# Kernel optimization log

Measured on AMD Instinct MI355X. Metric: run time of the kernel, lower is better.

Reference implementation:

```python
import jax, jax.numpy as jnp
import numpy as np

HEAD_NUM = 16
EMBED = 1024
B, T = 2, 2048


def setup_inputs() -> dict:
    key = jax.random.key(0)
    k1, k2, k3 = jax.random.split(key, 3)
    x = jax.random.normal(k1, (B, T, EMBED), dtype=jnp.float32)
    # torch Linear weights: [out_features, in_features]; scaled like default init
    w_qkv = jax.random.normal(k2, (3 * EMBED, EMBED), dtype=jnp.float32) / np.sqrt(EMBED)
    w_out = jax.random.normal(k3, (EMBED, EMBED), dtype=jnp.float32) / np.sqrt(EMBED)
    return {"x": x, "w_qkv": w_qkv, "w_out": w_out}


def reference(x, w_qkv, w_out):
    b, t, e = x.shape
    h = HEAD_NUM
    d = e // h
    dk = d ** 0.5  # NOTE: original MULTIPLIES scores by sqrt(head_dim)
    qkv = x @ w_qkv.T  # [b, t, 3e]
    # einops 'b t (d k h) -> k b h t d' with k=3: split order is (d, 3, h)
    qkv = qkv.reshape(b, t, d, 3, h)
    qkv = jnp.transpose(qkv, (3, 0, 4, 1, 2))  # [3, b, h, t, d]
    q, k, v = qkv[0], qkv[1], qkv[2]
    energy = jnp.einsum('bhid,bhjd->bhij', q, k) * dk  # [b, h, t, t]
    attn = jax.nn.softmax(energy, axis=-1)
    out = jnp.einsum('bhij,bhjd->bhid', attn, v)  # [b, h, t, d]
    out = jnp.transpose(out, (0, 2, 1, 3)).reshape(b, t, e)  # b t (h d)
    return out @ w_out.T
```

## Files before the change

kernel.cpp:

```cpp
#include <hip/hip_runtime.h>
#include <hip/hip_bf16.h>

typedef _Float16 f16x8 __attribute__((ext_vector_type(8)));
typedef unsigned short u16x8 __attribute__((ext_vector_type(8)));
typedef unsigned short u16x4 __attribute__((ext_vector_type(4)));
typedef float f32x4 __attribute__((ext_vector_type(4)));

static constexpr int Bn = 2;
static constexpr int Tn = 2048;
static constexpr int En = 1024;
static constexpr int Hn = 16;
static constexpr int Dn = 64;
#define LOG2E 1.44269504088896340736f

static constexpr int TS = 136;
static constexpr int PS = 40;

__device__ __forceinline__ unsigned short f2h(float x) {
  _Float16 h = (_Float16)x;
  return __builtin_bit_cast(unsigned short, h);
}
__device__ __forceinline__ float h2f(unsigned short u) {
  return (float)__builtin_bit_cast(_Float16, u);
}
__device__ __forceinline__ f16x8 ldh8(const unsigned short* p) {
  return __builtin_bit_cast(f16x8, *reinterpret_cast<const u16x8*>(p));
}
__device__ __forceinline__ unsigned int pk2(float a, float b) {
  return __builtin_bit_cast(unsigned int, __builtin_amdgcn_cvt_pkrtz(a, b));
}
__device__ __forceinline__ float fexp2(float x) {
  return __builtin_amdgcn_exp2f(x);
}
__device__ __forceinline__ void gld16(const void* g, void* l) {
  __builtin_amdgcn_global_load_lds(
      (__attribute__((address_space(1))) void*)(const_cast<void*>(g)),
      (__attribute__((address_space(3))) void*)(l), 16, 0, 0);
}

__global__ __launch_bounds__(256) void split_f32_f16(
    const float* __restrict__ src, unsigned short* __restrict__ hi,
    unsigned short* __restrict__ lo)
{
  const int i = (blockIdx.x * 256 + threadIdx.x) * 4;
  const float4 v = *reinterpret_cast<const float4*>(src + i);
  ushort4 h, l;
  h.x = f2h(v.x); l.x = f2h(v.x - h2f(h.x));
  h.y = f2h(v.y); l.y = f2h(v.y - h2f(h.y));
  h.z = f2h(v.z); l.z = f2h(v.z - h2f(h.z));
  h.w = f2h(v.w); l.w = f2h(v.w - h2f(h.w));
  *reinterpret_cast<ushort4*>(hi + i) = h;
  *reinterpret_cast<ushort4*>(lo + i) = l;
}

__global__ __launch_bounds__(256) void cvt_f32_f16(
    const float* __restrict__ src, unsigned short* __restrict__ dst)
{
  const int i = (blockIdx.x * 256 + threadIdx.x) * 4;
  const float4 v = *reinterpret_cast<const float4*>(src + i);
  ushort4 u;
  u.x = f2h(v.x); u.y = f2h(v.y); u.z = f2h(v.z); u.w = f2h(v.w);
  *reinterpret_cast<ushort4*>(dst + i) = u;
}

__global__ __launch_bounds__(256) void gemm_qkv(
    const unsigned short* __restrict__ xh, const unsigned short* __restrict__ xl,
    const unsigned short* __restrict__ wf,
    unsigned short* __restrict__ Qf, unsigned short* __restrict__ Kf,
    unsigned short* __restrict__ Vf, int M, int K)
{
  __shared__ unsigned short smem[2 * 12288];

  const int tid = threadIdx.x;
  const int w = tid >> 6, L = tid & 63, qd = L >> 4, lr = L & 15;
  const int m0 = blockIdx.y * 128;
  const int kk = blockIdx.x >> 3;
  const int hh0 = (blockIdx.x & 7) * 2;
  const int wm = (w >> 1) * 64, wn = (w & 1) * 64;

  size_t aoffs[2], boffs[2];
  int lbase[2];
#pragma unroll
  for (int p = 0; p < 2; ++p) {
    const int c = p * 256 + tid;
    const int row = c >> 2, slot = c & 3;
    const int dd = row & 63, hl = row >> 6;
    const int sg = slot ^ ((row >> 1) & 3);
    aoffs[p] = (size_t)(m0 + row) * K + sg * 8;
    boffs[p] = (size_t)(dd * 48 + kk * 16 + hh0 + hl) * K + sg * 8;
    lbase[p] = (p * 4 + w) * 512;
  }

  f32x4 acc[4][4] = {};

#pragma unroll
  for (int p = 0; p < 2; ++p) {
    gld16(xh + aoffs[p], &smem[lbase[p]]);
    gld16(wf + boffs[p], &smem[8192 + lbase[p]]);
    if (kk < 2) gld16(xl + aoffs[p], &smem[4096 + lbase[p]]);
  }
  __syncthreads();

  const int sw = (qd ^ ((lr >> 1) & 3)) * 8;

  int buf = 0;
  for (int k0 = 0; k0 < K; k0 += 32) {
    if (k0 + 32 < K) {
      const int nb = (buf ^ 1) * 12288;
#pragma unroll
      for (int p = 0; p < 2; ++p) {
        gld16(xh + aoffs[p] + k0 + 32, &smem[nb + lbase[p]]);
        gld16(wf + boffs[p] + k0 + 32, &smem[nb + 8192 + lbase[p]]);
        if (kk < 2) gld16(xl + aoffs[p] + k0 + 32, &smem[nb + 4096 + lbase[p]]);
      }
    }

    const int cb = buf * 12288;
    f16x8 afh[4], bf[4];
#pragma unroll
    for (int mt = 0; mt < 4; ++mt)
      afh[mt] = ldh8(&smem[cb + (wm + mt * 16 + lr) * 32 + sw]);
#pragma unroll
    for (int nt = 0; nt < 4; ++nt)
      bf[nt] = ldh8(&smem[cb + 8192 + (wn + nt * 16 + lr) * 32 + sw]);
    if (kk < 2) {
      f16x8 afl[4];
#pragma unroll
      for (int mt = 0; mt < 4; ++mt)
        afl[mt] = ldh8(&smem[cb + 4096 + (wm + mt * 16 + lr) * 32 + sw]);
#pragma unroll
      for (int mt = 0; mt < 4; ++mt)
#pragma unroll
        for (int nt = 0; nt < 4; ++nt) {
          acc[mt][nt] = __builtin_amdgcn_mfma_f32_16x16x32_f16(afh[mt], bf[nt], acc[mt][nt], 0, 0, 0);
          acc[mt][nt] = __builtin_amdgcn_mfma_f32_16x16x32_f16(afl[mt], bf[nt], acc[mt][nt], 0, 0, 0);
        }
    } else {
#pragma unroll
      for (int mt = 0; mt < 4; ++mt)
#pragma unroll
        for (int nt = 0; nt < 4; ++nt)
          acc[mt][nt] = __builtin_amdgcn_mfma_f32_16x16x32_f16(afh[mt], bf[nt], acc[mt][nt], 0, 0, 0);
    }
    __syncthreads();
    buf ^= 1;
  }

  const int b = m0 >> 11;
  const int t0 = m0 & (Tn - 1);
  const float qscale = (kk == 0) ? 8.0f * LOG2E : 1.0f;
#pragma unroll
  for (int mt = 0; mt < 4; ++mt)
#pragma unroll
    for (int nt = 0; nt < 4; ++nt)
#pragma unroll
      for (int r = 0; r < 4; ++r) {
        const int ml = wm + mt * 16 + qd * 4 + r;
        const int cl = wn + nt * 16 + lr;
        smem[ml * TS + cl] = f2h(acc[mt][nt][r] * qscale);
      }
  __syncthreads();

  unsigned short* dst = (kk == 0) ? Qf : (kk == 1) ? Kf : Vf;
  if (kk < 2) {
#pragma unroll
    for (int p = 0; p < 8; ++p) {
      const int s = p * 256 + tid;
      const int tl = s >> 4, sub = s & 15;
      const int hl = sub >> 3, oct = sub & 7;
      const u16x8 v = *reinterpret_cast<const u16x8*>(&smem[tl * TS + hl * 64 + oct * 8]);
      *reinterpret_cast<u16x8*>(
          dst + ((size_t)(b * Hn + hh0 + hl) * Tn + t0 + tl) * Dn + oct * 8) = v;
    }
  } else {
#pragma unroll
    for (int p = 0; p < 8; ++p) {
      const int s = p * 256 + tid;
      const int cl = s >> 4, oct = s & 15;
      const int hl = cl >> 6, dd = cl & 63;
      u16x8 v;
#pragma unroll
      for (int j = 0; j < 8; ++j) v[j] = smem[(oct * 8 + j) * TS + cl];
      *reinterpret_cast<u16x8*>(
          dst + ((size_t)((b * Hn + hh0 + hl) * Dn + dd)) * Tn + t0 + oct * 8) = v;
    }
  }
}

__global__ __launch_bounds__(256, 2) void attn_kernel(
    const unsigned short* __restrict__ Qf, const unsigned short* __restrict__ Kf,
    const unsigned short* __restrict__ Vf, unsigned short* __restrict__ AOf)
{
  __shared__ unsigned short shK[2 * 128 * 32];
  __shared__ unsigned short shV[4 * 64 * 32];
  __shared__ unsigned short shP[4 * 16 * PS];
  const int tid = threadIdx.x;
  const int w = tid >> 6, L = tid & 63, qd = L >> 4, lr = L & 15;
  const int q0 = blockIdx.x * 64;
  const int bh = blockIdx.y;
  unsigned short* myP = &shP[w * 16 * PS];

  f16x8 aq[2];
  {
    const size_t qoff = ((size_t)bh * Tn + q0 + w * 16 + lr) * Dn;
    aq[0] = ldh8(Qf + qoff + qd * 8);
    aq[1] = ldh8(Qf + qoff + 32 + qd * 8);
  }
  f16x8 ones;
#pragma unroll
  for (int j = 0; j < 8; ++j) ones[j] = (_Float16)1.0f;

  const int sw = (qd ^ ((lr >> 1) & 3)) * 8;

  f32x4 oacc[4] = {};
  float mrow = -1e30f, lsum = 0.f;

  for (int j0 = 0; j0 < Tn; j0 += 128) {
#pragma unroll
    for (int p = 0; p < 4; ++p) {
      const int kc = p >> 1, half = p & 1;
      const int row = half * 64 + (tid >> 2);
      const int slot = tid & 3;
      const int sg = slot ^ ((row >> 1) & 3);
      gld16(Kf + ((size_t)bh * Tn + j0 + row) * Dn + kc * 32 + sg * 8,
            &shK[kc * 4096 + (half * 64 + w * 16) * 32]);
    }
#pragma unroll
    for (int p = 0; p < 4; ++p) {
      const int dd = tid >> 2, slot = tid & 3;
      const int sg = slot ^ ((dd >> 1) & 3);
      gld16(Vf + ((size_t)bh * Dn + dd) * Tn + j0 + p * 32 + sg * 8,
            &shV[p * 2048 + (w * 16) * 32]);
    }
    __syncthreads();

    f32x4 s2[8];
#pragma unroll
    for (int ct = 0; ct < 8; ++ct) {
      const int rk = ct * 16 + lr;
      s2[ct] = f32x4{0.f, 0.f, 0.f, 0.f};
#pragma unroll
      for (int kc = 0; kc < 2; ++kc) {
        const f16x8 bk = ldh8(&shK[kc * 4096 + rk * 32 + sw]);
        s2[ct] = __builtin_amdgcn_mfma_f32_16x16x32_f16(bk, aq[kc], s2[ct], 0, 0, 0);
      }
    }

    float tm = s2[0][0];
#pragma unroll
    for (int ct = 0; ct < 8; ++ct)
#pragma unroll
      for (int r = 0; r < 4; ++r) tm = fmaxf(tm, s2[ct][r]);
    tm = fmaxf(tm, __shfl_xor(tm, 16, 64));
    tm = fmaxf(tm, __shfl_xor(tm, 32, 64));
    const float mn = fmaxf(mrow, tm);
    const float alpha = fexp2(mrow - mn);
    mrow = mn;
#pragma unroll
    for (int ct = 0; ct < 8; ++ct)
#pragma unroll
      for (int r = 0; r < 4; ++r)
        s2[ct][r] = fexp2(s2[ct][r] - mrow);
#pragma unroll
    for (int nt = 0; nt < 4; ++nt)
#pragma unroll
      for (int r = 0; r < 4; ++r) oacc[nt][r] *= alpha;

    f32x4 sacc = {};
#pragma unroll
    for (int kcv = 0; kcv < 4; ++kcv) {
#pragma unroll
      for (int c2 = 0; c2 < 2; ++c2) {
        const int ct = kcv * 2 + c2;
        uint2 d2;
        d2.x = pk2(s2[ct][0], s2[ct][1]);
        d2.y = pk2(s2[ct][2], s2[ct][3]);
        *reinterpret_cast<uint2*>(&myP[lr * PS + c2 * 16 + qd * 4]) = d2;
      }
      const f16x8 pa = ldh8(&myP[lr * PS + qd * 8]);
#pragma unroll
      for (int nt = 0; nt < 4; ++nt) {
        const int rv = nt * 16 + lr;
        const f16x8 bv = ldh8(&shV[kcv * 2048 + rv * 32 + sw]);
        oacc[nt] = __builtin_amdgcn_mfma_f32_16x16x32_f16(bv, pa, oacc[nt], 0, 0, 0);
      }
      sacc = __builtin_amdgcn_mfma_f32_16x16x32_f16(ones, pa, sacc, 0, 0, 0);
    }
    lsum = lsum * alpha + sacc[0];
    __syncthreads();
  }

  const int b = bh >> 4, h = bh & 15;
  const float inv = 1.0f / lsum;
  const int q = q0 + w * 16 + lr;
#pragma unroll
  for (int nt = 0; nt < 4; ++nt) {
    unsigned short o[4];
#pragma unroll
    for (int r = 0; r < 4; ++r) o[r] = f2h(oacc[nt][r] * inv);
    const int col = h * 64 + nt * 16 + qd * 4;
    *reinterpret_cast<u16x4*>(&AOf[((size_t)b * Tn + q) * En + col]) =
        u16x4{o[0], o[1], o[2], o[3]};
  }
}

__global__ __launch_bounds__(256) void gemm_out(
    const unsigned short* __restrict__ A, const unsigned short* __restrict__ Bm,
    float* __restrict__ C, int M, int N, int K)
{
  __shared__ unsigned short shA[128 * 32];
  __shared__ unsigned short shB[128 * 32];
  const int tid = threadIdx.x;
  const int w = tid >> 6, L = tid & 63, qd = L >> 4, lr = L & 15;
  const int m0 = blockIdx.y * 128;
  const int n0 = blockIdx.x * 128;
  const int wm = (w >> 1) * 64, wn = (w & 1) * 64;

  f32x4 acc[4][4] = {};

  for (int k0 = 0; k0 < K; k0 += 32) {
#pragma unroll
    for (int p = 0; p < 2; ++p) {
      const int c = p * 256 + tid;
      const int row = c >> 2, slot = c & 3;
      const int base = (p * 4 + w) * 512;
      gld16(A + (size_t)(m0 + row) * K + k0 + slot * 8, &shA[base]);
      gld16(Bm + (size_t)(n0 + row) * K + k0 + slot * 8, &shB[base]);
    }
    __syncthreads();

    f16x8 af[4], bf[4];
#pragma unroll
    for (int mt = 0; mt < 4; ++mt)
      af[mt] = ldh8(&shA[(wm + mt * 16 + lr) * 32 + qd * 8]);
#pragma unroll
    for (int nt = 0; nt < 4; ++nt)
      bf[nt] = ldh8(&shB[(wn + nt * 16 + lr) * 32 + qd * 8]);
#pragma unroll
    for (int mt = 0; mt < 4; ++mt)
#pragma unroll
      for (int nt = 0; nt < 4; ++nt)
        acc[mt][nt] = __builtin_amdgcn_mfma_f32_16x16x32_f16(af[mt], bf[nt], acc[mt][nt], 0, 0, 0);
    __syncthreads();
  }

#pragma unroll
  for (int mt = 0; mt < 4; ++mt)
#pragma unroll
    for (int nt = 0; nt < 4; ++nt)
#pragma unroll
      for (int r = 0; r < 4; ++r) {
        const int m = m0 + wm + mt * 16 + qd * 4 + r;
        const int n = n0 + wn + nt * 16 + lr;
        C[(size_t)m * N + n] = acc[mt][nt][r];
      }
}

extern "C" void kernel_launch(void* const* d_in, const int* in_sizes, int n_in,
                              void* d_out, int out_size, void* d_ws, size_t ws_size,
                              hipStream_t stream) {
  (void)in_sizes; (void)n_in; (void)out_size; (void)ws_size;
  const float* x = (const float*)d_in[0];
  const float* wqkv = (const float*)d_in[1];
  const float* wout = (const float*)d_in[2];
  float* out = (float*)d_out;

  const size_t elems = (size_t)Bn * Hn * Tn * Dn;
  unsigned short* Qf = (unsigned short*)d_ws;
  unsigned short* Kf = Qf + elems;
  unsigned short* Vf = Kf + elems;
  unsigned short* AOf = Vf + elems;
  unsigned short* wf = AOf + elems;
  unsigned short* wof = wf + (size_t)3 * En * En;

  unsigned short* xh = (unsigned short*)d_out;
  unsigned short* xl = xh + elems;

  const int M = Bn * Tn;
  dim3 blk(256);
  split_f32_f16<<<dim3((int)(elems / 1024)), blk, 0, stream>>>(x, xh, xl);
  cvt_f32_f16<<<dim3(3 * En * En / 1024), blk, 0, stream>>>(wqkv, wf);
  cvt_f32_f16<<<dim3(En * En / 1024), blk, 0, stream>>>(wout, wof);
  gemm_qkv<<<dim3(24, M / 128), blk, 0, stream>>>(
      xh, xl, wf, Qf, Kf, Vf, M, En);
  attn_kernel<<<dim3(Tn / 64, Bn * Hn), blk, 0, stream>>>(Qf, Kf, Vf, AOf);
  gemm_out<<<dim3(En / 128, M / 128), blk, 0, stream>>>(
      AOf, wof, out, M, En, En);
}
```

Measured before the change: 233.1 us.

## Double-buffer output GEMM with swizzled LDS and unroll QKV loop by two

The output projection GEMM goes from a single-buffered load-sync-compute loop to a double-buffered LDS pipeline, so global-to-LDS copies for the next K slice overlap the MFMA work on the current one. Its LDS layout also gets the same XOR swizzle as the QKV GEMM to reduce bank conflicts. The QKV GEMM loop is unrolled by two with constant buffer offsets, which removes the runtime buffer index. Both loops now assume K is a multiple of 64, and the output GEMM uses twice the shared memory.

```diff
diff --git a/kernel.cpp b/kernel.cpp
--- a/kernel.cpp
+++ b/kernel.cpp
@@ -93,29 +93,17 @@
 
   f32x4 acc[4][4] = {};
 
-#pragma unroll
-  for (int p = 0; p < 2; ++p) {
-    gld16(xh + aoffs[p], &smem[lbase[p]]);
-    gld16(wf + boffs[p], &smem[8192 + lbase[p]]);
-    if (kk < 2) gld16(xl + aoffs[p], &smem[4096 + lbase[p]]);
-  }
-  __syncthreads();
-
   const int sw = (qd ^ ((lr >> 1) & 3)) * 8;
 
-  int buf = 0;
-  for (int k0 = 0; k0 < K; k0 += 32) {
-    if (k0 + 32 < K) {
-      const int nb = (buf ^ 1) * 12288;
-#pragma unroll
-      for (int p = 0; p < 2; ++p) {
-        gld16(xh + aoffs[p] + k0 + 32, &smem[nb + lbase[p]]);
-        gld16(wf + boffs[p] + k0 + 32, &smem[nb + 8192 + lbase[p]]);
-        if (kk < 2) gld16(xl + aoffs[p] + k0 + 32, &smem[nb + 4096 + lbase[p]]);
-      }
-    }
-
-    const int cb = buf * 12288;
+  auto stage = [&](int k0s, int bufbase) {
+#pragma unroll
+    for (int p = 0; p < 2; ++p) {
+      gld16(xh + aoffs[p] + k0s, &smem[bufbase + lbase[p]]);
+      gld16(wf + boffs[p] + k0s, &smem[bufbase + 8192 + lbase[p]]);
+      if (kk < 2) gld16(xl + aoffs[p] + k0s, &smem[bufbase + 4096 + lbase[p]]);
+    }
+  };
+  auto compute = [&](int cb) {
     f16x8 afh[4], bf[4];
 #pragma unroll
     for (int mt = 0; mt < 4; ++mt)
@@ -142,8 +130,18 @@
         for (int nt = 0; nt < 4; ++nt)
           acc[mt][nt] = __builtin_amdgcn_mfma_f32_16x16x32_f16(afh[mt], bf[nt], acc[mt][nt], 0, 0, 0);
     }
-    __syncthreads();
-    buf ^= 1;
+  };
+
+  stage(0, 0);
+  __syncthreads();
+
+  for (int k0 = 0; k0 < K; k0 += 64) {
+    if (k0 + 32 < K) stage(k0 + 32, 12288);
+    compute(0);
+    __syncthreads();
+    if (k0 + 64 < K) stage(k0 + 64, 0);
+    compute(12288);
+    __syncthreads();
   }
 
   const int b = m0 >> 11;
@@ -308,39 +306,59 @@
     const unsigned short* __restrict__ A, const unsigned short* __restrict__ Bm,
     float* __restrict__ C, int M, int N, int K)
 {
-  __shared__ unsigned short shA[128 * 32];
-  __shared__ unsigned short shB[128 * 32];
+  __shared__ unsigned short smem[2 * 8192];
   const int tid = threadIdx.x;
   const int w = tid >> 6, L = tid & 63, qd = L >> 4, lr = L & 15;
   const int m0 = blockIdx.y * 128;
   const int n0 = blockIdx.x * 128;
   const int wm = (w >> 1) * 64, wn = (w & 1) * 64;
 
+  size_t aoffs[2], boffs[2];
+  int lbase[2];
+#pragma unroll
+  for (int p = 0; p < 2; ++p) {
+    const int c = p * 256 + tid;
+    const int row = c >> 2, slot = c & 3;
+    const int sg = slot ^ ((row >> 1) & 3);
+    aoffs[p] = (size_t)(m0 + row) * K + sg * 8;
+    boffs[p] = (size_t)(n0 + row) * K + sg * 8;
+    lbase[p] = (p * 4 + w) * 512;
+  }
+  const int sw = (qd ^ ((lr >> 1) & 3)) * 8;
+
   f32x4 acc[4][4] = {};
 
-  for (int k0 = 0; k0 < K; k0 += 32) {
+  auto stage = [&](int k0s, int bufbase) {
 #pragma unroll
     for (int p = 0; p < 2; ++p) {
-      const int c = p * 256 + tid;
-      const int row = c >> 2, slot = c & 3;
-      const int base = (p * 4 + w) * 512;
-      gld16(A + (size_t)(m0 + row) * K + k0 + slot * 8, &shA[base]);
-      gld16(Bm + (size_t)(n0 + row) * K + k0 + slot * 8, &shB[base]);
-    }
-    __syncthreads();
-
+      gld16(A + aoffs[p] + k0s, &smem[bufbase + lbase[p]]);
+      gld16(Bm + boffs[p] + k0s, &smem[bufbase + 4096 + lbase[p]]);
+    }
+  };
+  auto compute = [&](int cb) {
     f16x8 af[4], bf[4];
 #pragma unroll
     for (int mt = 0; mt < 4; ++mt)
-      af[mt] = ldh8(&shA[(wm + mt * 16 + lr) * 32 + qd * 8]);
+      af[mt] = ldh8(&smem[cb + (wm + mt * 16 + lr) * 32 + sw]);
 #pragma unroll
     for (int nt = 0; nt < 4; ++nt)
-      bf[nt] = ldh8(&shB[(wn + nt * 16 + lr) * 32 + qd * 8]);
+      bf[nt] = ldh8(&smem[cb + 4096 + (wn + nt * 16 + lr) * 32 + sw]);
 #pragma unroll
     for (int mt = 0; mt < 4; ++mt)
 #pragma unroll
       for (int nt = 0; nt < 4; ++nt)
         acc[mt][nt] = __builtin_amdgcn_mfma_f32_16x16x32_f16(af[mt], bf[nt], acc[mt][nt], 0, 0, 0);
+  };
+
+  stage(0, 0);
+  __syncthreads();
+
+  for (int k0 = 0; k0 < K; k0 += 64) {
+    if (k0 + 32 < K) stage(k0 + 32, 8192);
+    compute(0);
+    __syncthreads();
+    if (k0 + 64 < K) stage(k0 + 64, 0);
+    compute(8192);
     __syncthreads();
   }
 
```

Result: slower. 241.3 us (+3.5%).
